# Performance work log

Measured on AMD Instinct MI355X. Metric: run time of the kernel, lower is better.

Reference implementation:

```python
import jax, jax.numpy as jnp
import numpy as np

HS = 1024
IMS = 4096
NHEAD = 16
EPS = 1e-5


def _layer_norm(x, g, b):
    mu = jnp.mean(x, axis=-1, keepdims=True)
    var = jnp.mean(jnp.square(x - mu), axis=-1, keepdims=True)
    return (x - mu) * jax.lax.rsqrt(var + EPS) * g + b


def setup_inputs() -> dict:
    key = jax.random.key(0)
    ks = jax.random.split(key, 10)
    B, S = 16, 512
    x = jax.random.normal(ks[0], (B, S, HS), dtype=jnp.float32)
    input_mask = jnp.zeros((B, S), dtype=jnp.float32)  # additive mask, 0 = attend
    sc = 0.02
    return {
        "x": x,
        "input_mask": input_mask,
        "qkv_w": jax.random.normal(ks[1], (3 * HS, HS), jnp.float32) * sc,
        "qkv_b": jnp.zeros((3 * HS,), jnp.float32),
        "attn_ow": jax.random.normal(ks[2], (HS, HS), jnp.float32) * sc,
        "attn_ob": jnp.zeros((HS,), jnp.float32),
        "ln1_g": jnp.ones((HS,), jnp.float32),
        "ln1_b": jnp.zeros((HS,), jnp.float32),
        "inter_w": jax.random.normal(ks[3], (IMS, HS), jnp.float32) * sc,
        "inter_b": jnp.zeros((IMS,), jnp.float32),
        "out_w": jax.random.normal(ks[4], (HS, IMS), jnp.float32) * sc,
        "out_b": jnp.zeros((HS,), jnp.float32),
        "ln2_g": jnp.ones((HS,), jnp.float32),
        "ln2_b": jnp.zeros((HS,), jnp.float32),
    }


def reference(x, input_mask, qkv_w, qkv_b, attn_ow, attn_ob, ln1_g, ln1_b,
              inter_w, inter_b, out_w, out_b, ln2_g, ln2_b):
    B, S, H = x.shape
    d = H // NHEAD
    # ---- self-attention block (pre_layer_norm=True, eval mode => no dropout) ----
    resid = x
    y = _layer_norm(x, ln1_g, ln1_b)
    qkv = jnp.einsum('bsh,eh->bse', y, qkv_w) + qkv_b  # [B,S,3H]
    q, k, v = jnp.split(qkv, 3, axis=-1)
    q = q.reshape(B, S, NHEAD, d)
    k = k.reshape(B, S, NHEAD, d)
    v = v.reshape(B, S, NHEAD, d)
    scores = jnp.einsum('bqnd,bknd->bnqk', q, k) / jnp.sqrt(jnp.float32(d))
    scores = scores + input_mask[:, None, None, :]  # additive padding mask
    probs = jax.nn.softmax(scores, axis=-1)
    ctx = jnp.einsum('bnqk,bknd->bqnd', probs, v).reshape(B, S, H)
    attn_out = jnp.einsum('bsh,oh->bso', ctx, attn_ow) + attn_ob
    x = resid + attn_out
    # ---- FFN block ----
    resid = x
    y = _layer_norm(x, ln2_g, ln2_b)
    h = jax.nn.relu(jnp.einsum('bsh,ih->bsi', y, inter_w) + inter_b)
    ffn_out = jnp.einsum('bsi,oi->bso', h, out_w) + out_b
    return resid + ffn_out
```

## Files before the change

kernel.cpp:

```cpp
#include <hip/hip_runtime.h>


using f32x4  = __attribute__((ext_vector_type(4))) float;
using f32x16 = __attribute__((ext_vector_type(16))) float;
using s16x8  = __attribute__((ext_vector_type(8))) short;
using i32x4  = __attribute__((ext_vector_type(4))) int;

__device__ __forceinline__ unsigned short f2bf(float f) {
    unsigned x = __builtin_bit_cast(unsigned, f);
    return (unsigned short)((x + 0x7fffu + ((x >> 16) & 1u)) >> 16);
}

#define GLL16(gptr, lptr)                                                     \
    __builtin_amdgcn_global_load_lds(                                         \
        (const __attribute__((address_space(1))) void*)(gptr),                \
        (__attribute__((address_space(3))) void*)(lptr), 16, 0, 0)

#define VMC(N) asm volatile("s_waitcnt vmcnt(" #N ")" ::: "memory")

__global__ __launch_bounds__(256) void wconv_kernel(
    const float* __restrict__ w0, const float* __restrict__ w1,
    const float* __restrict__ w2, const float* __restrict__ w3,
    unsigned short* __restrict__ o0, unsigned short* __restrict__ o1,
    unsigned short* __restrict__ o2, unsigned short* __restrict__ o3) {
    long idx = (long)blockIdx.x * 256 + threadIdx.x;
    const float* src;
    unsigned short* dst;
    long rel;
    if (idx < 786432L)        { src = w0; dst = o0; rel = idx; }
    else if (idx < 1048576L)  { src = w1; dst = o1; rel = idx - 786432L; }
    else if (idx < 2097152L)  { src = w2; dst = o2; rel = idx - 1048576L; }
    else                      { src = w3; dst = o3; rel = idx - 2097152L; }
    float4 v = *(const float4*)(src + rel * 4);
    ushort4 o;
    o.x = f2bf(v.x); o.y = f2bf(v.y); o.z = f2bf(v.z); o.w = f2bf(v.w);
    *(ushort4*)(dst + rel * 4) = o;
}

__global__ __launch_bounds__(256) void ln_kernel(
    const float* __restrict__ x, const float* __restrict__ gw,
    const float* __restrict__ bw, unsigned short* __restrict__ y) {
    __shared__ float rbuf[8];
    const int row = blockIdx.x;
    const int t = threadIdx.x;
    const float* xr = x + (size_t)row * 1024;
    float4 v = *(const float4*)(xr + t * 4);
    float s  = v.x + v.y + v.z + v.w;
    float ss = v.x * v.x + v.y * v.y + v.z * v.z + v.w * v.w;
#pragma unroll
    for (int sh = 1; sh < 64; sh <<= 1) {
        s  += __shfl_xor(s, sh, 64);
        ss += __shfl_xor(ss, sh, 64);
    }
    int w = t >> 6;
    if ((t & 63) == 0) { rbuf[w * 2] = s; rbuf[w * 2 + 1] = ss; }
    __syncthreads();
    s  = rbuf[0] + rbuf[2] + rbuf[4] + rbuf[6];
    ss = rbuf[1] + rbuf[3] + rbuf[5] + rbuf[7];
    float mu  = s * (1.f / 1024.f);
    float var = ss * (1.f / 1024.f) - mu * mu;
    float rs  = rsqrtf(var + 1e-5f);
    float4 gv = *(const float4*)(gw + t * 4);
    float4 bv = *(const float4*)(bw + t * 4);
    ushort4 o;
    o.x = f2bf((v.x - mu) * rs * gv.x + bv.x);
    o.y = f2bf((v.y - mu) * rs * gv.y + bv.y);
    o.z = f2bf((v.z - mu) * rs * gv.z + bv.z);
    o.w = f2bf((v.w - mu) * rs * gv.w + bv.w);
    *(ushort4*)(y + (size_t)row * 1024 + t * 4) = o;
}

template <bool RELU, bool RESID, bool OUT_BF16>
__global__ __launch_bounds__(256, 2) void gemm_bt(
    const unsigned short* __restrict__ A, const unsigned short* __restrict__ Bw,
    const float* __restrict__ bias, const float* __restrict__ resid,
    void* __restrict__ Cout, int M, int N, int K) {
    __shared__ char smem[2 * 128 * 64 * 2];
    char* As = smem;
    char* Bs = smem + 128 * 64 * 2;

    const int tid = threadIdx.x;
    const int lane = tid & 63;
    const int w = tid >> 6;
    const int wr = w >> 1, wc = w & 1;
    const int g = lane >> 4;
    const int fr = lane & 15;
    const int nwg = gridDim.x * gridDim.y;
    const int L = blockIdx.y * gridDim.x + blockIdx.x;
    const int swz = (L & 7) * (nwg >> 3) + (L >> 3);
    const int m0 = (swz / gridDim.x) * 128;
    const int n0 = (swz % gridDim.x) * 128;

    f32x4 acc[4][4] = {};

    for (int kt = 0; kt < K; kt += 64) {
#pragma unroll
        for (int c = 0; c < 4; ++c) {
            int lin = (c * 256 + tid) * 16;
            int row = lin >> 7;
            int Lb = lin ^ ((row & 7) << 4);
            int colb = Lb & 127;
            const char* ga = (const char*)A + ((size_t)(m0 + row) * K + kt) * 2 + colb;
            const char* gb = (const char*)Bw + ((size_t)(n0 + row) * K + kt) * 2 + colb;
            GLL16(ga, As + lin);
            GLL16(gb, Bs + lin);
        }
        __syncthreads();
#pragma unroll
        for (int ks = 0; ks < 2; ++ks) {
            s16x8 af[4], bf[4];
#pragma unroll
            for (int mi = 0; mi < 4; ++mi) {
                int row = wr * 64 + mi * 16 + fr;
                int off = (row << 7) + ((ks * 64 + g * 16) ^ ((row & 7) << 4));
                af[mi] = *(const s16x8*)(As + off);
            }
#pragma unroll
            for (int ni = 0; ni < 4; ++ni) {
                int row = wc * 64 + ni * 16 + fr;
                int off = (row << 7) + ((ks * 64 + g * 16) ^ ((row & 7) << 4));
                bf[ni] = *(const s16x8*)(Bs + off);
            }
#pragma unroll
            for (int mi = 0; mi < 4; ++mi)
#pragma unroll
                for (int ni = 0; ni < 4; ++ni)
                    acc[mi][ni] = __builtin_amdgcn_mfma_f32_16x16x32_bf16(
                        af[mi], bf[ni], acc[mi][ni], 0, 0, 0);
        }
        __syncthreads();
    }

    float bv[4];
#pragma unroll
    for (int ni = 0; ni < 4; ++ni) bv[ni] = bias[n0 + wc * 64 + ni * 16 + fr];
#pragma unroll
    for (int mi = 0; mi < 4; ++mi) {
#pragma unroll
        for (int r = 0; r < 4; ++r) {
            int row = m0 + wr * 64 + mi * 16 + g * 4 + r;
#pragma unroll
            for (int ni = 0; ni < 4; ++ni) {
                int col = n0 + wc * 64 + ni * 16 + fr;
                float v = acc[mi][ni][r] + bv[ni];
                if (RELU) v = v > 0.f ? v : 0.f;
                if (RESID) v += resid[(size_t)row * N + col];
                if (OUT_BF16)
                    ((unsigned short*)Cout)[(size_t)row * N + col] = f2bf(v);
                else
                    ((float*)Cout)[(size_t)row * N + col] = v;
            }
        }
    }
}

template <bool RELU, bool OUT_BF16>
__global__ __launch_bounds__(512, 2) void gemm256(
    const unsigned short* __restrict__ A, const unsigned short* __restrict__ Bw,
    const float* __restrict__ bias, void* __restrict__ Cout,
    int M, int N, int K) {
    extern __shared__ char lds[];

    const int tid = threadIdx.x;
    const int lane = tid & 63;
    const int w = tid >> 6;
    const int wm = w >> 2, wn = w & 3;
    const int g = lane >> 4, fr = lane & 15;

    const int nwg = gridDim.x * gridDim.y;
    const int L = blockIdx.y * gridDim.x + blockIdx.x;
    const int swz = (L & 7) * (nwg >> 3) + (L >> 3);
    const int m0 = (swz / gridDim.x) * 256;
    const int n0 = (swz % gridDim.x) * 256;

    const int NT = K >> 6;

    auto stageA = [&](int t, int h) {
        char* dst = lds + (t & 1) * 32768 + h * 16384;
#pragma unroll
        for (int c2 = 0; c2 < 2; ++c2) {
            int lin = (c2 * 512 + tid) * 16;
            int row = lin >> 7;
            int colb = (lin & 127) ^ ((row & 7) << 4);
            GLL16((const char*)A + ((size_t)(m0 + h * 128 + row) * K + t * 64) * 2 + colb,
                  dst + lin);
        }
    };
    auto stageB = [&](int t, int h) {
        char* dst = lds + 65536 + (t & 1) * 32768 + h * 16384;
#pragma unroll
        for (int c2 = 0; c2 < 2; ++c2) {
            int lin = (c2 * 512 + tid) * 16;
            int row = lin >> 7;
            int colb = (lin & 127) ^ ((row & 7) << 4);
            GLL16((const char*)Bw + ((size_t)(n0 + h * 128 + row) * K + t * 64) * 2 + colb,
                  dst + lin);
        }
    };

    f32x4 acc[2][4][2][2] = {};
    s16x8 af[4][2];
    s16x8 bf[2][2];

    auto loadA = [&](const char* Ab, int ha) {
#pragma unroll
        for (int mi2 = 0; mi2 < 4; ++mi2) {
            int row = ha * 128 + wm * 64 + mi2 * 16 + fr;
#pragma unroll
            for (int ks = 0; ks < 2; ++ks)
                af[mi2][ks] = *(const s16x8*)(Ab + (row << 7) +
                               ((ks * 64 + g * 16) ^ ((row & 7) << 4)));
        }
    };
    auto loadB = [&](const char* Bb, int hb) {
#pragma unroll
        for (int ni2 = 0; ni2 < 2; ++ni2) {
            int row = hb * 128 + wn * 32 + ni2 * 16 + fr;
#pragma unroll
            for (int ks = 0; ks < 2; ++ks)
                bf[ni2][ks] = *(const s16x8*)(Bb + (row << 7) +
                               ((ks * 64 + g * 16) ^ ((row & 7) << 4)));
        }
    };

#define MFMAQ(HA, HB)                                                         \
    __builtin_amdgcn_s_barrier();                                             \
    asm volatile("s_waitcnt lgkmcnt(0)" ::: "memory");                        \
    __builtin_amdgcn_sched_barrier(0);                                        \
    __builtin_amdgcn_s_setprio(1);                                            \
    _Pragma("unroll")                                                         \
    for (int mi2 = 0; mi2 < 4; ++mi2)                                         \
        _Pragma("unroll")                                                     \
        for (int ni2 = 0; ni2 < 2; ++ni2)                                     \
            _Pragma("unroll")                                                 \
            for (int ks = 0; ks < 2; ++ks)                                    \
                acc[HA][mi2][HB][ni2] =                                       \
                    __builtin_amdgcn_mfma_f32_16x16x32_bf16(                  \
                        af[mi2][ks], bf[ni2][ks], acc[HA][mi2][HB][ni2],      \
                        0, 0, 0);                                             \
    __builtin_amdgcn_s_setprio(0);                                            \
    __builtin_amdgcn_s_barrier();

    stageA(0, 0); stageB(0, 0); stageA(0, 1); stageB(0, 1);
    stageA(1, 0); stageB(1, 0);
    VMC(8);
    __builtin_amdgcn_s_barrier();

    for (int t = 0; t < NT - 2; ++t) {
        char* Ab = lds + (t & 1) * 32768;
        char* Bb = lds + 65536 + (t & 1) * 32768;
        loadA(Ab, 0); loadB(Bb, 0); stageA(t + 1, 1); VMC(6); MFMAQ(0, 0);
        loadB(Bb, 1);               stageB(t + 1, 1);         MFMAQ(0, 1);
        loadA(Ab, 1); loadB(Bb, 0); stageA(t + 2, 0);         MFMAQ(1, 0);
        loadB(Bb, 1);               stageB(t + 2, 0); VMC(8); MFMAQ(1, 1);
    }
    {
        const int t = NT - 2;
        char* Ab = lds + (t & 1) * 32768;
        char* Bb = lds + 65536 + (t & 1) * 32768;
        loadA(Ab, 0); loadB(Bb, 0); stageA(t + 1, 1); VMC(6); MFMAQ(0, 0);
        loadB(Bb, 1);               stageB(t + 1, 1);         MFMAQ(0, 1);
        loadA(Ab, 1); loadB(Bb, 0);                           MFMAQ(1, 0);
        loadB(Bb, 1);                                 VMC(4); MFMAQ(1, 1);
    }
    {
        const int t = NT - 1;
        char* Ab = lds + (t & 1) * 32768;
        char* Bb = lds + 65536 + (t & 1) * 32768;
        loadA(Ab, 0); loadB(Bb, 0);                   VMC(0); MFMAQ(0, 0);
        loadB(Bb, 1);                                         MFMAQ(0, 1);
        loadA(Ab, 1); loadB(Bb, 0);                           MFMAQ(1, 0);
        loadB(Bb, 1);                                         MFMAQ(1, 1);
    }
#undef MFMAQ

#pragma unroll
    for (int ha = 0; ha < 2; ++ha)
#pragma unroll
        for (int mi2 = 0; mi2 < 4; ++mi2)
#pragma unroll
            for (int r = 0; r < 4; ++r) {
                int row = m0 + ha * 128 + wm * 64 + mi2 * 16 + g * 4 + r;
#pragma unroll
                for (int hb = 0; hb < 2; ++hb)
#pragma unroll
                    for (int ni2 = 0; ni2 < 2; ++ni2) {
                        int col = n0 + hb * 128 + wn * 32 + ni2 * 16 + fr;
                        float v = acc[ha][mi2][hb][ni2][r] + bias[col];
                        if (RELU) v = v > 0.f ? v : 0.f;
                        if (OUT_BF16)
                            ((unsigned short*)Cout)[(size_t)row * N + col] = f2bf(v);
                        else
                            ((float*)Cout)[(size_t)row * N + col] = v;
                    }
            }
}

__global__ __launch_bounds__(512, 2) void attn_kernel(
    const unsigned short* __restrict__ qkv, const float* __restrict__ mask,
    unsigned short* __restrict__ ctx) {
    extern __shared__ char smem[];

    const int tid = threadIdx.x;
    const int lane = tid & 63;
    const int w = tid >> 6;
    const int l31 = lane & 31;
    const int hi = lane >> 5;
    const int bh = blockIdx.x >> 1;
    const int b = bh >> 4, h = bh & 15;
    const int qt = (blockIdx.x & 1) * 256 + w * 32;

    const size_t rstr = 3072;
    const unsigned short* qbase = qkv + (size_t)b * 512 * rstr + h * 64;
    const unsigned short* kbase = qbase + 1024;
    const unsigned short* vbase = qbase + 2048;
    const float* mrow = mask + b * 512;

    s16x8 qf[4];
#pragma unroll
    for (int kc = 0; kc < 4; ++kc)
        qf[kc] = *(const s16x8*)(qbase + (size_t)(qt + l31) * rstr + kc * 16 + hi * 8);

    f32x16 O0 = {}, O1 = {};
    float m = -3e38f, l = 0.f;
    const int bpbase = 36 * hi * 4;

    auto stage = [&](int kt, int bufsel) {
        char* Kb = smem + bufsel * 16384;
        char* Vb = smem + 32768 + bufsel * 16384;
#pragma unroll
        for (int c = 0; c < 2; ++c) {
            int lin = (c * 512 + tid) * 16;
            int row = lin >> 7;
            int colb = (lin & 127) ^ ((row & 7) << 4);
            GLL16((const char*)kbase + (size_t)(kt * 128 + row) * rstr * 2 + colb,
                  Kb + lin);
        }
        int s = tid & 127, dg = tid >> 7;
        const unsigned short* vsrc = vbase + (size_t)(kt * 128 + s) * rstr + dg * 16;
        union { i32x4 v; unsigned short u[8]; } v0, v1;
        v0.v = *(const i32x4*)vsrc;
        v1.v = *(const i32x4*)(vsrc + 8);
#pragma unroll
        for (int j = 0; j < 8; ++j) {
            int d = dg * 16 + j;
            *(unsigned short*)(Vb + d * 256 + ((s * 2) ^ ((d & 15) << 4))) = v0.u[j];
        }
#pragma unroll
        for (int j = 0; j < 8; ++j) {
            int d = dg * 16 + 8 + j;
            *(unsigned short*)(Vb + d * 256 + ((s * 2) ^ ((d & 15) << 4))) = v1.u[j];
        }
    };

    const float C   = 0.18033688f;
    const float L2E = 1.44269504f;

    stage(0, 0);
    __syncthreads();

    for (int kt = 0; kt < 4; ++kt) {
        const int cur = kt & 1;
        if (kt < 3) stage(kt + 1, cur ^ 1);
        char* Kb = smem + cur * 16384;
        char* Vb = smem + 32768 + cur * 16384;
        const int swzk = (l31 & 7) << 4;

        f32x16 sc[4];
#pragma unroll
        for (int t = 0; t < 4; ++t) {
            f32x16 a = {};
#pragma unroll
            for (int kc = 0; kc < 4; ++kc) {
                s16x8 kf = *(const s16x8*)(Kb + (32 * t + l31) * 128 +
                                           ((kc * 32 + hi * 16) ^ swzk));
                a = __builtin_amdgcn_mfma_f32_32x32x16_bf16(kf, qf[kc], a, 0, 0, 0);
            }
            sc[t] = a;
        }

        float tm = -3e38f;
#pragma unroll
        for (int t = 0; t < 4; ++t) {
#pragma unroll
            for (int k2 = 0; k2 < 4; ++k2) {
                f32x4 mk = *(const f32x4*)(mrow + kt * 128 + 32 * t + 8 * k2 + 4 * hi);
#pragma unroll
                for (int i = 0; i < 4; ++i) {
                    float v = sc[t][4 * k2 + i] * C + mk[i] * L2E;
                    sc[t][4 * k2 + i] = v;
                    tm = fmaxf(tm, v);
                }
            }
        }
        tm = fmaxf(tm, __shfl_xor(tm, 32, 64));

        if (__any(tm > m + 11.0f)) {
            float mn = fmaxf(m, tm);
            float fac = exp2f(m - mn);
            m = mn;
            l *= fac;
            int fi = __float_as_int(fac);
#pragma unroll
            for (int r = 0; r < 16; ++r) {
                int q2 = (r & 3) + 8 * (r >> 2);
                float fq = __int_as_float(
                    __builtin_amdgcn_ds_bpermute(bpbase + q2 * 4, fi));
                O0[r] *= fq;
                O1[r] *= fq;
            }
        }

        float ts = 0.f;
#pragma unroll
        for (int t = 0; t < 4; ++t)
#pragma unroll
            for (int r = 0; r < 16; ++r) {
                float p = exp2f(sc[t][r] - m);
                sc[t][r] = p;
                ts += p;
            }
        ts += __shfl_xor(ts, 32, 64);
        l += ts;

        unsigned pk01[4][4], pk23[4][4];
#pragma unroll
        for (int t = 0; t < 4; ++t)
#pragma unroll
            for (int k = 0; k < 4; ++k) {
                unsigned r0, r1;
                asm("v_cvt_pk_bf16_f32 %0, %1, %2"
                    : "=v"(r0) : "v"(sc[t][4 * k]), "v"(sc[t][4 * k + 1]));
                asm("v_cvt_pk_bf16_f32 %0, %1, %2"
                    : "=v"(r1) : "v"(sc[t][4 * k + 2]), "v"(sc[t][4 * k + 3]));
                pk01[t][k] = r0;
                pk23[t][k] = r1;
            }

#pragma unroll
        for (int t = 0; t < 4; ++t)
#pragma unroll
            for (int cc = 0; cc < 2; ++cc) {
                unsigned a0 = pk01[t][2 * cc], b0 = pk01[t][2 * cc + 1];
                unsigned c0 = pk23[t][2 * cc], d0 = pk23[t][2 * cc + 1];
                asm("v_permlane32_swap_b32 %0, %1" : "+v"(a0), "+v"(b0));
                asm("v_permlane32_swap_b32 %0, %1" : "+v"(c0), "+v"(d0));
                union { unsigned u[4]; s16x8 v; } pf;
                pf.u[0] = a0;
                pf.u[1] = c0;
                pf.u[2] = b0;
                pf.u[3] = d0;
                const int kc = 2 * t + cc;
                {
                    int row = l31;
                    s16x8 vf = *(const s16x8*)(Vb + row * 256 +
                               ((kc * 32 + hi * 16) ^ ((row & 15) << 4)));
                    O0 = __builtin_amdgcn_mfma_f32_32x32x16_bf16(pf.v, vf, O0, 0, 0, 0);
                }
                {
                    int row = 32 + l31;
                    s16x8 vf = *(const s16x8*)(Vb + row * 256 +
                               ((kc * 32 + hi * 16) ^ ((row & 15) << 4)));
                    O1 = __builtin_amdgcn_mfma_f32_32x32x16_bf16(pf.v, vf, O1, 0, 0, 0);
                }
            }
        __syncthreads();
    }

    const int li = __float_as_int(l);
#pragma unroll
    for (int r = 0; r < 16; ++r) {
        int q2 = (r & 3) + 8 * (r >> 2);
        float lq = __int_as_float(__builtin_amdgcn_ds_bpermute(bpbase + q2 * 4, li));
        float inv = 1.f / lq;
        size_t rowg = (size_t)(b * 512 + qt + q2 + 4 * hi) * 1024 + h * 64;
        ctx[rowg + l31]      = f2bf(O0[r] * inv);
        ctx[rowg + 32 + l31] = f2bf(O1[r] * inv);
    }
}

extern "C" void kernel_launch(void* const* d_in, const int* in_sizes, int n_in,
                              void* d_out, int out_size, void* d_ws, size_t ws_size,
                              hipStream_t stream) {
    const float* x    = (const float*)d_in[0];
    const float* mask = (const float*)d_in[1];
    const float* qkvw = (const float*)d_in[2];
    const float* qkvb = (const float*)d_in[3];
    const float* ow   = (const float*)d_in[4];
    const float* ob   = (const float*)d_in[5];
    const float* ln1g = (const float*)d_in[6];
    const float* ln1b = (const float*)d_in[7];
    const float* iw   = (const float*)d_in[8];
    const float* ib   = (const float*)d_in[9];
    const float* o2w  = (const float*)d_in[10];
    const float* o2b  = (const float*)d_in[11];
    const float* ln2g = (const float*)d_in[12];
    const float* ln2b = (const float*)d_in[13];

    char* ws = (char*)d_ws;
    unsigned short* qkvbuf = (unsigned short*)(ws);
    unsigned short* ybuf   = (unsigned short*)(ws + 50331648);
    unsigned short* cbuf   = (unsigned short*)(ws + 67108864);
    float*          x2     = (float*)(ws + 83886080);
    unsigned short* wq     = (unsigned short*)(ws + 117440512);
    unsigned short* wo     = (unsigned short*)(ws + 123731968);
    unsigned short* wi     = (unsigned short*)(ws + 125829120);
    unsigned short* wo2    = (unsigned short*)(ws + 134217728);
    unsigned short* hbuf   = (unsigned short*)(ws);

    hipFuncSetAttribute(reinterpret_cast<const void*>(attn_kernel),
                        hipFuncAttributeMaxDynamicSharedMemorySize, 65536);
    hipFuncSetAttribute(reinterpret_cast<const void*>(&gemm256<false, true>),
                        hipFuncAttributeMaxDynamicSharedMemorySize, 131072);
    hipFuncSetAttribute(reinterpret_cast<const void*>(&gemm256<true, true>),
                        hipFuncAttributeMaxDynamicSharedMemorySize, 131072);

    wconv_kernel<<<12288, 256, 0, stream>>>(qkvw, ow, iw, o2w, wq, wo, wi, wo2);
    ln_kernel<<<8192, 256, 0, stream>>>(x, ln1g, ln1b, ybuf);
    gemm256<false, true><<<dim3(12, 32), 512, 131072, stream>>>(
        ybuf, wq, qkvb, qkvbuf, 8192, 3072, 1024);
    attn_kernel<<<512, 512, 65536, stream>>>(qkvbuf, mask, cbuf);
    gemm_bt<false, true, false><<<dim3(8, 64), 256, 0, stream>>>(
        cbuf, wo, ob, x, x2, 8192, 1024, 1024);
    ln_kernel<<<8192, 256, 0, stream>>>(x2, ln2g, ln2b, cbuf);
    gemm256<true, true><<<dim3(16, 32), 512, 131072, stream>>>(
        cbuf, wi, ib, hbuf, 8192, 4096, 1024);
    gemm_bt<false, true, false><<<dim3(8, 64), 256, 0, stream>>>(
        hbuf, wo2, o2b, x2, (float*)d_out, 8192, 1024, 4096);
}
```

Baseline: 307.8 us.

## Store mid-residual in bf16, use 128-tile GEMM for QKV, defer V LDS writes

The intermediate residual x2 is now stored as bf16 instead of fp32. The second LayerNorm and the final GEMM residual add read it as bf16, which cuts memory traffic but lowers the precision of the residual path. The QKV projection moves from the 256-tile gemm256 kernel to the 128-tile gemm_bt kernel with a larger grid. In attention, the V global loads are issued early into registers and written to LDS after the softmax, to overlap load latency with compute at the cost of extra live registers.

Measured after the change: 291.9 us. 5.2% less time.

```diff
diff --git a/kernel.cpp b/kernel.cpp
--- a/kernel.cpp
+++ b/kernel.cpp
@@ -9,6 +9,9 @@
 __device__ __forceinline__ unsigned short f2bf(float f) {
     unsigned x = __builtin_bit_cast(unsigned, f);
     return (unsigned short)((x + 0x7fffu + ((x >> 16) & 1u)) >> 16);
+}
+__device__ __forceinline__ float bf2f(unsigned short u) {
+    return __builtin_bit_cast(float, (unsigned)u << 16);
 }
 
 #define GLL16(gptr, lptr)                                                     \
@@ -37,14 +40,21 @@
     *(ushort4*)(dst + rel * 4) = o;
 }
 
+template <bool IN_BF16>
 __global__ __launch_bounds__(256) void ln_kernel(
-    const float* __restrict__ x, const float* __restrict__ gw,
+    const void* __restrict__ xin, const float* __restrict__ gw,
     const float* __restrict__ bw, unsigned short* __restrict__ y) {
     __shared__ float rbuf[8];
     const int row = blockIdx.x;
     const int t = threadIdx.x;
-    const float* xr = x + (size_t)row * 1024;
-    float4 v = *(const float4*)(xr + t * 4);
+    float4 v;
+    if (IN_BF16) {
+        ushort4 u = *(const ushort4*)((const unsigned short*)xin +
+                                      (size_t)row * 1024 + t * 4);
+        v.x = bf2f(u.x); v.y = bf2f(u.y); v.z = bf2f(u.z); v.w = bf2f(u.w);
+    } else {
+        v = *(const float4*)((const float*)xin + (size_t)row * 1024 + t * 4);
+    }
     float s  = v.x + v.y + v.z + v.w;
     float ss = v.x * v.x + v.y * v.y + v.z * v.z + v.w * v.w;
 #pragma unroll
@@ -70,10 +80,10 @@
     *(ushort4*)(y + (size_t)row * 1024 + t * 4) = o;
 }
 
-template <bool RELU, bool RESID, bool OUT_BF16>
+template <bool RELU, bool RESID, bool RESID_BF16, bool OUT_BF16>
 __global__ __launch_bounds__(256, 2) void gemm_bt(
     const unsigned short* __restrict__ A, const unsigned short* __restrict__ Bw,
-    const float* __restrict__ bias, const float* __restrict__ resid,
+    const float* __restrict__ bias, const void* __restrict__ resid,
     void* __restrict__ Cout, int M, int N, int K) {
     __shared__ char smem[2 * 128 * 64 * 2];
     char* As = smem;
@@ -144,7 +154,11 @@
                 int col = n0 + wc * 64 + ni * 16 + fr;
                 float v = acc[mi][ni][r] + bv[ni];
                 if (RELU) v = v > 0.f ? v : 0.f;
-                if (RESID) v += resid[(size_t)row * N + col];
+                if (RESID) {
+                    size_t ri = (size_t)row * N + col;
+                    v += RESID_BF16 ? bf2f(((const unsigned short*)resid)[ri])
+                                    : ((const float*)resid)[ri];
+                }
                 if (OUT_BF16)
                     ((unsigned short*)Cout)[(size_t)row * N + col] = f2bf(v);
                 else
@@ -325,9 +339,16 @@
     float m = -3e38f, l = 0.f;
     const int bpbase = 36 * hi * 4;
 
-    auto stage = [&](int kt, int bufsel) {
+    const int vs = tid & 127, vdg = tid >> 7;
+    i32x4 vr0, vr1;
+
+    auto issueV = [&](int kt) {
+        const unsigned short* vsrc = vbase + (size_t)(kt * 128 + vs) * rstr + vdg * 16;
+        vr0 = *(const i32x4*)vsrc;
+        vr1 = *(const i32x4*)(vsrc + 8);
+    };
+    auto issueK = [&](int kt, int bufsel) {
         char* Kb = smem + bufsel * 16384;
-        char* Vb = smem + 32768 + bufsel * 16384;
 #pragma unroll
         for (int c = 0; c < 2; ++c) {
             int lin = (c * 512 + tid) * 16;
@@ -336,32 +357,33 @@
             GLL16((const char*)kbase + (size_t)(kt * 128 + row) * rstr * 2 + colb,
                   Kb + lin);
         }
-        int s = tid & 127, dg = tid >> 7;
-        const unsigned short* vsrc = vbase + (size_t)(kt * 128 + s) * rstr + dg * 16;
-        union { i32x4 v; unsigned short u[8]; } v0, v1;
-        v0.v = *(const i32x4*)vsrc;
-        v1.v = *(const i32x4*)(vsrc + 8);
+    };
+    auto writeV = [&](int bufsel) {
+        char* Vb = smem + 32768 + bufsel * 16384;
+        union { i32x4 v; unsigned short u[8]; } u0, u1;
+        u0.v = vr0; u1.v = vr1;
 #pragma unroll
         for (int j = 0; j < 8; ++j) {
-            int d = dg * 16 + j;
-            *(unsigned short*)(Vb + d * 256 + ((s * 2) ^ ((d & 15) << 4))) = v0.u[j];
+            int d = vdg * 16 + j;
+            *(unsigned short*)(Vb + d * 256 + ((vs * 2) ^ ((d & 15) << 4))) = u0.u[j];
         }
 #pragma unroll
         for (int j = 0; j < 8; ++j) {
-            int d = dg * 16 + 8 + j;
-            *(unsigned short*)(Vb + d * 256 + ((s * 2) ^ ((d & 15) << 4))) = v1.u[j];
+            int d = vdg * 16 + 8 + j;
+            *(unsigned short*)(Vb + d * 256 + ((vs * 2) ^ ((d & 15) << 4))) = u1.u[j];
         }
     };
 
     const float C   = 0.18033688f;
     const float L2E = 1.44269504f;
 
-    stage(0, 0);
+    issueV(0); issueK(0, 0);
+    writeV(0);
     __syncthreads();
 
     for (int kt = 0; kt < 4; ++kt) {
         const int cur = kt & 1;
-        if (kt < 3) stage(kt + 1, cur ^ 1);
+        if (kt < 3) { issueV(kt + 1); issueK(kt + 1, cur ^ 1); }
         char* Kb = smem + cur * 16384;
         char* Vb = smem + 32768 + cur * 16384;
         const int swzk = (l31 & 7) << 4;
@@ -422,6 +444,8 @@
             }
         ts += __shfl_xor(ts, 32, 64);
         l += ts;
+
+        if (kt < 3) writeV(cur ^ 1);
 
         unsigned pk01[4][4], pk23[4][4];
 #pragma unroll
@@ -501,7 +525,7 @@
     unsigned short* qkvbuf = (unsigned short*)(ws);
     unsigned short* ybuf   = (unsigned short*)(ws + 50331648);
     unsigned short* cbuf   = (unsigned short*)(ws + 67108864);
-    float*          x2     = (float*)(ws + 83886080);
+    unsigned short* x2bf   = (unsigned short*)(ws + 83886080);
     unsigned short* wq     = (unsigned short*)(ws + 117440512);
     unsigned short* wo     = (unsigned short*)(ws + 123731968);
     unsigned short* wi     = (unsigned short*)(ws + 125829120);
@@ -510,21 +534,19 @@
 
     hipFuncSetAttribute(reinterpret_cast<const void*>(attn_kernel),
                         hipFuncAttributeMaxDynamicSharedMemorySize, 65536);
-    hipFuncSetAttribute(reinterpret_cast<const void*>(&gemm256<false, true>),
-                        hipFuncAttributeMaxDynamicSharedMemorySize, 131072);
     hipFuncSetAttribute(reinterpret_cast<const void*>(&gemm256<true, true>),
                         hipFuncAttributeMaxDynamicSharedMemorySize, 131072);
 
     wconv_kernel<<<12288, 256, 0, stream>>>(qkvw, ow, iw, o2w, wq, wo, wi, wo2);
-    ln_kernel<<<8192, 256, 0, stream>>>(x, ln1g, ln1b, ybuf);
-    gemm256<false, true><<<dim3(12, 32), 512, 131072, stream>>>(
-        ybuf, wq, qkvb, qkvbuf, 8192, 3072, 1024);
+    ln_kernel<false><<<8192, 256, 0, stream>>>(x, ln1g, ln1b, ybuf);
+    gemm_bt<false, false, false, true><<<dim3(24, 64), 256, 0, stream>>>(
+        ybuf, wq, qkvb, nullptr, qkvbuf, 8192, 3072, 1024);
     attn_kernel<<<512, 512, 65536, stream>>>(qkvbuf, mask, cbuf);
-    gemm_bt<false, true, false><<<dim3(8, 64), 256, 0, stream>>>(
-        cbuf, wo, ob, x, x2, 8192, 1024, 1024);
-    ln_kernel<<<8192, 256, 0, stream>>>(x2, ln2g, ln2b, cbuf);
+    gemm_bt<false, true, false, true><<<dim3(8, 64), 256, 0, stream>>>(
+        cbuf, wo, ob, x, x2bf, 8192, 1024, 1024);
+    ln_kernel<true><<<8192, 256, 0, stream>>>(x2bf, ln2g, ln2b, cbuf);
     gemm256<true, true><<<dim3(16, 32), 512, 131072, stream>>>(
         cbuf, wi, ib, hbuf, 8192, 4096, 1024);
-    gemm_bt<false, true, false><<<dim3(8, 64), 256, 0, stream>>>(
-        hbuf, wo2, o2b, x2, (float*)d_out, 8192, 1024, 4096);
-}
+    gemm_bt<false, true, true, false><<<dim3(8, 64), 256, 0, stream>>>(
+        hbuf, wo2, o2b, x2bf, (float*)d_out, 8192, 1024, 4096);
+}
```
